# Kernel tuning notes

Hardware: AMD Instinct MI355X
Metric: run time of the kernel (lower is better)

The kernel has to match this reference:

```python
import jax, jax.numpy as jnp
import numpy as np

B, H, S, D = 4, 16, 2048, 64
TEMPERATURE = 8.0  # sqrt(D)
NEG = -1000000000.0

def setup_inputs() -> dict:
    key = jax.random.key(0)
    kq, kk, kv, km = jax.random.split(key, 4)
    q = jax.random.normal(kq, (B, H, S, D), dtype=jnp.float32)
    k = jax.random.normal(kk, (B, H, S, D), dtype=jnp.float32)
    v = jax.random.normal(kv, (B, H, S, D), dtype=jnp.float32)
    mask = jax.random.randint(km, (B, 1, S, S), 0, 2, dtype=jnp.int32)
    return {"q": q, "k": k, "v": v, "mask": mask}

def reference(q, k, v, mask):
    # scores: [B,H,S,S]
    scores = jnp.einsum('bhqd,bhkd->bhqk', q / TEMPERATURE, k)
    scores = jnp.where(mask == 1, NEG, scores)
    attn = jax.nn.softmax(scores, axis=-1)  # dropout p=0.0 -> identity
    out = jnp.einsum('bhqk,bhkd->bhqd', attn, v)
    return out
```

## Files before the change

### kernel.cpp

```cpp
#include <hip/hip_runtime.h>

#define NB 4
#define NH 16
#define SS 2048
#define DD 64
#define QT 128
#define KT 64
#define NT (SS / KT)
#define KSP 72
#define VSP 72
#define QSCALE 0.18033688011112042f
#define MASK_BITS_BYTES ((size_t)NB * SS * (SS / 8))

typedef __bf16 bf16x8 __attribute__((ext_vector_type(8)));
typedef __bf16 bf16x2 __attribute__((ext_vector_type(2)));
typedef float  floatx16 __attribute__((ext_vector_type(16)));
typedef unsigned long long u64t;

static_assert(sizeof(bf16x8) == 16, "bf16x8 must be 16B");

__device__ __forceinline__ int pack2(float a, float b) {
    bf16x2 v; v[0] = (__bf16)a; v[1] = (__bf16)b;
    return __builtin_bit_cast(int, v);
}

__global__ __launch_bounds__(256)
void pack_mask_kernel(const int* __restrict__ M, u64t* __restrict__ bits)
{
    const int w    = (blockIdx.x * 256 + threadIdx.x) >> 6;
    const int lane = threadIdx.x & 63;
    #pragma unroll 4
    for (int i = 0; i < 32; ++i) {
        const int gw   = i * 8192 + w;
        const size_t row = (size_t)(gw >> 5);
        const int word = gw & 31;
        const int mval = M[row * SS + (size_t)word * 64 + lane];
        const u64t b = __ballot(mval == 1);
        if (lane == 0) bits[gw] = b;
    }
}

template<bool USE_BITS>
__global__ __launch_bounds__(256, 4)
void attn_kernel(const float* __restrict__ Q, const float* __restrict__ K,
                 const float* __restrict__ V, const int* __restrict__ M,
                 const unsigned* __restrict__ MB, float* __restrict__ O)
{
    __shared__ __bf16 ks [2][KT][KSP];
    __shared__ __bf16 vsT[2][DD][VSP];

    const int t    = threadIdx.x;
    const int wave = t >> 6;
    const int lane = t & 63;
    const int l31  = lane & 31;
    const int h8   = lane >> 5;

    const int bh    = blockIdx.x & 63;
    const int qtile = blockIdx.x >> 6;
    const int b     = bh >> 4;
    const int q0    = qtile * QT + wave * 32;

    const size_t base = (size_t)bh * SS * DD;
    const float* Qb = Q + base;
    const float* Kb = K + base;
    const float* Vb = V + base;

    bf16x8 aq[4];
    {
        const float* qp = Qb + (size_t)(q0 + l31) * DD + 8 * h8;
        #pragma unroll
        for (int s = 0; s < 4; ++s) {
            float4 f0 = *(const float4*)(qp + 16 * s);
            float4 f1 = *(const float4*)(qp + 16 * s + 4);
            bf16x8 a;
            a[0] = (__bf16)(f0.x * QSCALE); a[1] = (__bf16)(f0.y * QSCALE);
            a[2] = (__bf16)(f0.z * QSCALE); a[3] = (__bf16)(f0.w * QSCALE);
            a[4] = (__bf16)(f1.x * QSCALE); a[5] = (__bf16)(f1.y * QSCALE);
            a[6] = (__bf16)(f1.z * QSCALE); a[7] = (__bf16)(f1.w * QSCALE);
            aq[s] = a;
        }
    }

    const int skey = t >> 3;
    const int sdc  = (t & 7) * 8;
    const int vk   = 2 * (t & 15);
    const int vdc  = (t >> 4) * 4;
    const int vcol = 16 * (vk >> 4) + 8 * ((vk >> 2) & 1) + (vk & 3) + 4 * ((vk >> 3) & 1);

    const float* kp0 = Kb + (size_t)skey * DD + sdc;
    const float* vp0 = Vb + (size_t)vk * DD + vdc;

    float4 ka0 = ((const float4*)kp0)[0];
    float4 ka1 = ((const float4*)kp0)[1];
    float4 kb0 = ((const float4*)(kp0 + 32 * DD))[0];
    float4 kb1 = ((const float4*)(kp0 + 32 * DD))[1];
    float4 va0 = *(const float4*)(vp0);
    float4 va1 = *(const float4*)(vp0 + DD);
    float4 vb0 = *(const float4*)(vp0 + 32 * DD);
    float4 vb1 = *(const float4*)(vp0 + 33 * DD);

    const u64t* mbrow = (const u64t*)MB + ((size_t)b * SS + q0 + l31) * (SS / 64);
    const int*  mrow  = M + (size_t)b * SS * SS + (size_t)(q0 + l31) * SS + 4 * h8;

    floatx16 o0, o1;
    #pragma unroll
    for (int i = 0; i < 16; ++i) { o0[i] = 0.f; o1[i] = 0.f; }
    float ls = 0.f;

    for (int tt = 0; tt < NT; ++tt) {
        const int cur = tt & 1;

        {
            bf16x8 kw;
            kw[0]=(__bf16)ka0.x; kw[1]=(__bf16)ka0.y; kw[2]=(__bf16)ka0.z; kw[3]=(__bf16)ka0.w;
            kw[4]=(__bf16)ka1.x; kw[5]=(__bf16)ka1.y; kw[6]=(__bf16)ka1.z; kw[7]=(__bf16)ka1.w;
            *(bf16x8*)&ks[cur][skey][sdc] = kw;
            kw[0]=(__bf16)kb0.x; kw[1]=(__bf16)kb0.y; kw[2]=(__bf16)kb0.z; kw[3]=(__bf16)kb0.w;
            kw[4]=(__bf16)kb1.x; kw[5]=(__bf16)kb1.y; kw[6]=(__bf16)kb1.z; kw[7]=(__bf16)kb1.w;
            *(bf16x8*)&ks[cur][skey + 32][sdc] = kw;
            #pragma unroll
            for (int i = 0; i < 4; ++i) {
                bf16x2 pr;
                pr[0] = (__bf16)(&va0.x)[i]; pr[1] = (__bf16)(&va1.x)[i];
                *(bf16x2*)&vsT[cur][vdc + i][vcol] = pr;
                pr[0] = (__bf16)(&vb0.x)[i]; pr[1] = (__bf16)(&vb1.x)[i];
                *(bf16x2*)&vsT[cur][vdc + i][32 + vcol] = pr;
            }
        }
        __syncthreads();

        u64t mall = 0;
        int4 mi[8];
        if (USE_BITS) {
            mall = mbrow[tt];
        } else {
            #pragma unroll
            for (int g = 0; g < 8; ++g)
                mi[g] = *(const int4*)(mrow + tt * KT + 8 * g);
        }

        {
            const int jn = ((tt + 1) * KT) & (SS - 1);
            const float* kn = kp0 + (size_t)jn * DD;
            ka0 = ((const float4*)kn)[0];
            ka1 = ((const float4*)kn)[1];
            kb0 = ((const float4*)(kn + 32 * DD))[0];
            kb1 = ((const float4*)(kn + 32 * DD))[1];
            const float* vn = vp0 + (size_t)jn * DD;
            va0 = *(const float4*)(vn);
            va1 = *(const float4*)(vn + DD);
            vb0 = *(const float4*)(vn + 32 * DD);
            vb1 = *(const float4*)(vn + 33 * DD);
        }

        #pragma unroll
        for (int half = 0; half < 2; ++half) {
            floatx16 c;
            #pragma unroll
            for (int i = 0; i < 16; ++i) c[i] = 0.f;
            __builtin_amdgcn_s_setprio(1);
            #pragma unroll
            for (int s = 0; s < 4; ++s) {
                bf16x8 a = *(const bf16x8*)&ks[cur][32 * half + l31][16 * s + 8 * h8];
                c = __builtin_amdgcn_mfma_f32_32x32x16_bf16(a, aq[s], c, 0, 0, 0);
            }
            __builtin_amdgcn_s_setprio(0);

            const unsigned mw = USE_BITS ? (unsigned)(mall >> (32 * half)) : 0u;
            const unsigned u  = mw >> (4 * h8);
            int pk[8];
            float psum = 0.f;
            #pragma unroll
            for (int g = 0; g < 8; ++g) {
                const int ia = 2 * g, ib = 2 * g + 1;
                float pa = __builtin_amdgcn_exp2f(c[ia]);
                float pb = __builtin_amdgcn_exp2f(c[ib]);
                bool ma, mb_;
                if (USE_BITS) {
                    ma  = (u >> ((ia & 3) + 8 * (ia >> 2))) & 1;
                    mb_ = (u >> ((ib & 3) + 8 * (ib >> 2))) & 1;
                } else {
                    const int g2 = 4 * half + (ia >> 2);
                    ma  = ((&mi[g2].x)[ia & 3] == 1);
                    mb_ = ((&mi[g2].x)[ib & 3] == 1);
                }
                pa = ma  ? 0.f : pa;
                pb = mb_ ? 0.f : pb;
                psum += pa + pb;
                pk[g] = pack2(pa, pb);
            }
            ls += psum;

            __builtin_amdgcn_s_setprio(1);
            #pragma unroll
            for (int s2 = 0; s2 < 2; ++s2) {
                int4 fw; fw.x = pk[4*s2]; fw.y = pk[4*s2+1]; fw.z = pk[4*s2+2]; fw.w = pk[4*s2+3];
                bf16x8 bp = __builtin_bit_cast(bf16x8, fw);
                bf16x8 av0 = *(const bf16x8*)&vsT[cur][l31][32 * half + 16 * s2 + 8 * h8];
                bf16x8 av1 = *(const bf16x8*)&vsT[cur][32 + l31][32 * half + 16 * s2 + 8 * h8];
                o0 = __builtin_amdgcn_mfma_f32_32x32x16_bf16(av0, bp, o0, 0, 0, 0);
                o1 = __builtin_amdgcn_mfma_f32_32x32x16_bf16(av1, bp, o1, 0, 0, 0);
            }
            __builtin_amdgcn_s_setprio(0);
        }
    }

    ls += __shfl_xor(ls, 32);
    float inv = 1.0f / ls;
    float* op = O + base + (size_t)(q0 + l31) * DD;
    #pragma unroll
    for (int s = 0; s < 4; ++s) {
        float4 st0, st1;
        st0.x = o0[4*s+0] * inv; st0.y = o0[4*s+1] * inv;
        st0.z = o0[4*s+2] * inv; st0.w = o0[4*s+3] * inv;
        st1.x = o1[4*s+0] * inv; st1.y = o1[4*s+1] * inv;
        st1.z = o1[4*s+2] * inv; st1.w = o1[4*s+3] * inv;
        *(float4*)(op + 8 * s + 4 * h8)      = st0;
        *(float4*)(op + 32 + 8 * s + 4 * h8) = st1;
    }
}

extern "C" void kernel_launch(void* const* d_in, const int* in_sizes, int n_in,
                              void* d_out, int out_size, void* d_ws, size_t ws_size,
                              hipStream_t stream) {
    (void)in_sizes; (void)n_in; (void)out_size;
    const float* q = (const float*)d_in[0];
    const float* k = (const float*)d_in[1];
    const float* v = (const float*)d_in[2];
    const int*   m = (const int*)d_in[3];
    float* out = (float*)d_out;
    dim3 grid(NB * NH * (SS / QT));

    if (ws_size >= MASK_BITS_BYTES) {
        u64t* bits = (u64t*)d_ws;
        pack_mask_kernel<<<dim3(2048), 256, 0, stream>>>(m, bits);
        attn_kernel<true><<<grid, 256, 0, stream>>>(q, k, v, m, (const unsigned*)bits, out);
    } else {
        attn_kernel<false><<<grid, 256, 0, stream>>>(q, k, v, m, (const unsigned*)nullptr, out);
    }
}
```

Before: 281.0 us.

## Use 512-thread blocks with 256-query tiles and XOR-swizzled LDS layout

Doubles the query tile per block to 8 waves, so each K/V tile staged in LDS is shared by twice as many waves and each thread loads half as much K/V per iteration. The padded LDS arrays are replaced by unpadded ones with an XOR swizzle on 16-byte chunks, which keeps bank conflicts low while using less shared memory. The trade-offs are half as many blocks in the grid, larger blocks that may lower occupancy, and extra address arithmetic for the swizzle.

Measured after the change: 261.1 us. 7.1% less time.

```diff
diff --git a/kernel.cpp b/kernel.cpp
--- a/kernel.cpp
+++ b/kernel.cpp
@@ -4,11 +4,9 @@
 #define NH 16
 #define SS 2048
 #define DD 64
-#define QT 128
+#define QT 256
 #define KT 64
 #define NT (SS / KT)
-#define KSP 72
-#define VSP 72
 #define QSCALE 0.18033688011112042f
 #define MASK_BITS_BYTES ((size_t)NB * SS * (SS / 8))
 
@@ -41,13 +39,13 @@
 }
 
 template<bool USE_BITS>
-__global__ __launch_bounds__(256, 4)
+__global__ __launch_bounds__(512, 4)
 void attn_kernel(const float* __restrict__ Q, const float* __restrict__ K,
                  const float* __restrict__ V, const int* __restrict__ M,
                  const unsigned* __restrict__ MB, float* __restrict__ O)
 {
-    __shared__ __bf16 ks [2][KT][KSP];
-    __shared__ __bf16 vsT[2][DD][VSP];
+    __shared__ __bf16 ks [2][KT][DD];
+    __shared__ __bf16 vsT[2][DD][KT];
 
     const int t    = threadIdx.x;
     const int wave = t >> 6;
@@ -83,8 +81,8 @@
 
     const int skey = t >> 3;
     const int sdc  = (t & 7) * 8;
-    const int vk   = 2 * (t & 15);
-    const int vdc  = (t >> 4) * 4;
+    const int vk   = 2 * (t & 31);
+    const int vdc  = (t >> 5) * 4;
     const int vcol = 16 * (vk >> 4) + 8 * ((vk >> 2) & 1) + (vk & 3) + 4 * ((vk >> 3) & 1);
 
     const float* kp0 = Kb + (size_t)skey * DD + sdc;
@@ -92,12 +90,8 @@
 
     float4 ka0 = ((const float4*)kp0)[0];
     float4 ka1 = ((const float4*)kp0)[1];
-    float4 kb0 = ((const float4*)(kp0 + 32 * DD))[0];
-    float4 kb1 = ((const float4*)(kp0 + 32 * DD))[1];
     float4 va0 = *(const float4*)(vp0);
     float4 va1 = *(const float4*)(vp0 + DD);
-    float4 vb0 = *(const float4*)(vp0 + 32 * DD);
-    float4 vb1 = *(const float4*)(vp0 + 33 * DD);
 
     const u64t* mbrow = (const u64t*)MB + ((size_t)b * SS + q0 + l31) * (SS / 64);
     const int*  mrow  = M + (size_t)b * SS * SS + (size_t)(q0 + l31) * SS + 4 * h8;
@@ -109,22 +103,20 @@
 
     for (int tt = 0; tt < NT; ++tt) {
         const int cur = tt & 1;
+        char* kb = (char*)&ks[cur][0][0];
+        char* vb = (char*)&vsT[cur][0][0];
 
         {
             bf16x8 kw;
             kw[0]=(__bf16)ka0.x; kw[1]=(__bf16)ka0.y; kw[2]=(__bf16)ka0.z; kw[3]=(__bf16)ka0.w;
             kw[4]=(__bf16)ka1.x; kw[5]=(__bf16)ka1.y; kw[6]=(__bf16)ka1.z; kw[7]=(__bf16)ka1.w;
-            *(bf16x8*)&ks[cur][skey][sdc] = kw;
-            kw[0]=(__bf16)kb0.x; kw[1]=(__bf16)kb0.y; kw[2]=(__bf16)kb0.z; kw[3]=(__bf16)kb0.w;
-            kw[4]=(__bf16)kb1.x; kw[5]=(__bf16)kb1.y; kw[6]=(__bf16)kb1.z; kw[7]=(__bf16)kb1.w;
-            *(bf16x8*)&ks[cur][skey + 32][sdc] = kw;
+            *(bf16x8*)(kb + skey * 128 + ((16 * (t & 7)) ^ ((skey & 7) << 4))) = kw;
             #pragma unroll
             for (int i = 0; i < 4; ++i) {
                 bf16x2 pr;
                 pr[0] = (__bf16)(&va0.x)[i]; pr[1] = (__bf16)(&va1.x)[i];
-                *(bf16x2*)&vsT[cur][vdc + i][vcol] = pr;
-                pr[0] = (__bf16)(&vb0.x)[i]; pr[1] = (__bf16)(&vb1.x)[i];
-                *(bf16x2*)&vsT[cur][vdc + i][32 + vcol] = pr;
+                const int dim = vdc + i;
+                *(bf16x2*)(vb + dim * 128 + ((2 * vcol) ^ ((dim & 7) << 4))) = pr;
             }
         }
         __syncthreads();
@@ -144,13 +136,9 @@
             const float* kn = kp0 + (size_t)jn * DD;
             ka0 = ((const float4*)kn)[0];
             ka1 = ((const float4*)kn)[1];
-            kb0 = ((const float4*)(kn + 32 * DD))[0];
-            kb1 = ((const float4*)(kn + 32 * DD))[1];
             const float* vn = vp0 + (size_t)jn * DD;
             va0 = *(const float4*)(vn);
             va1 = *(const float4*)(vn + DD);
-            vb0 = *(const float4*)(vn + 32 * DD);
-            vb1 = *(const float4*)(vn + 33 * DD);
         }
 
         #pragma unroll
@@ -161,7 +149,9 @@
             __builtin_amdgcn_s_setprio(1);
             #pragma unroll
             for (int s = 0; s < 4; ++s) {
-                bf16x8 a = *(const bf16x8*)&ks[cur][32 * half + l31][16 * s + 8 * h8];
+                const int r = 32 * half + l31;
+                bf16x8 a = *(const bf16x8*)(kb + r * 128 +
+                              ((32 * s + 16 * h8) ^ ((r & 7) << 4)));
                 c = __builtin_amdgcn_mfma_f32_32x32x16_bf16(a, aq[s], c, 0, 0, 0);
             }
             __builtin_amdgcn_s_setprio(0);
@@ -196,8 +186,11 @@
             for (int s2 = 0; s2 < 2; ++s2) {
                 int4 fw; fw.x = pk[4*s2]; fw.y = pk[4*s2+1]; fw.z = pk[4*s2+2]; fw.w = pk[4*s2+3];
                 bf16x8 bp = __builtin_bit_cast(bf16x8, fw);
-                bf16x8 av0 = *(const bf16x8*)&vsT[cur][l31][32 * half + 16 * s2 + 8 * h8];
-                bf16x8 av1 = *(const bf16x8*)&vsT[cur][32 + l31][32 * half + 16 * s2 + 8 * h8];
+                const int c2 = 64 * half + 32 * s2 + 16 * h8;
+                bf16x8 av0 = *(const bf16x8*)(vb + l31 * 128 +
+                               (c2 ^ ((l31 & 7) << 4)));
+                bf16x8 av1 = *(const bf16x8*)(vb + (32 + l31) * 128 +
+                               (c2 ^ ((l31 & 7) << 4)));
                 o0 = __builtin_amdgcn_mfma_f32_32x32x16_bf16(av0, bp, o0, 0, 0, 0);
                 o1 = __builtin_amdgcn_mfma_f32_32x32x16_bf16(av1, bp, o1, 0, 0, 0);
             }
@@ -234,8 +227,8 @@
     if (ws_size >= MASK_BITS_BYTES) {
         u64t* bits = (u64t*)d_ws;
         pack_mask_kernel<<<dim3(2048), 256, 0, stream>>>(m, bits);
-        attn_kernel<true><<<grid, 256, 0, stream>>>(q, k, v, m, (const unsigned*)bits, out);
+        attn_kernel<true><<<grid, 512, 0, stream>>>(q, k, v, m, (const unsigned*)bits, out);
     } else {
-        attn_kernel<false><<<grid, 256, 0, stream>>>(q, k, v, m, (const unsigned*)nullptr, out);
-    }
-}
+        attn_kernel<false><<<grid, 512, 0, stream>>>(q, k, v, m, (const unsigned*)nullptr, out);
+    }
+}
```
